# Kernel optimization log

Measured on AMD Instinct MI355X. Metric: run time of the kernel, lower is better.

The kernel has to match this reference:

```python
import jax, jax.numpy as jnp
import numpy as np

HASHMAP_SIZES = [65536, 262144]
HASHMAP_DIM = 4
RESO = 2097152
OUTPUT_DIM = 48


def setup_inputs() -> dict:
    key = jax.random.key(0)
    k1, k2, k3, k4 = jax.random.split(key, 4)
    total = sum(HASHMAP_SIZES)
    # codes initialized uniform(-1, 1) as in torch.nn.init.uniform_
    codes = jax.random.uniform(k1, (total, HASHMAP_DIM), dtype=jnp.float32, minval=-1.0, maxval=1.0)
    # bias-free linear head: stored as [in, out] so forward is feats @ W
    fan_in = len(HASHMAP_SIZES) * HASHMAP_DIM
    W = jax.random.normal(k2, (fan_in, OUTPUT_DIM), dtype=jnp.float32) / np.sqrt(fan_in)
    map_65536 = jax.random.randint(k3, (RESO, HASHMAP_DIM), 0, 65536, dtype=jnp.int64) if jax.config.jax_enable_x64 else jax.random.randint(k3, (RESO, HASHMAP_DIM), 0, 65536, dtype=jnp.int32)
    map_262144 = jax.random.randint(k4, (RESO, HASHMAP_DIM), 0, 262144, dtype=jnp.int32)
    return {"codes": codes, "W": W, "map_65536": map_65536, "map_262144": map_262144}


def _gather_level(code, idx_map):
    # code: [size, dim]; idx_map: [reso, dim]; out[n, i] = code[idx_map[n, i], i]
    dim_idx = jnp.arange(code.shape[1])[None, :]  # [1, dim]
    return code[idx_map, dim_idx]  # [reso, dim]


def reference(codes, W, map_65536, map_262144):
    # split stacked codebook into per-level tables
    code0 = codes[: HASHMAP_SIZES[0]]                      # [65536, 4]
    code1 = codes[HASHMAP_SIZES[0] : HASHMAP_SIZES[0] + HASHMAP_SIZES[1]]  # [262144, 4]
    out0 = _gather_level(code0, map_65536)    # [RESO, 4]
    out1 = _gather_level(code1, map_262144)   # [RESO, 4]
    feats = jnp.concatenate([out0, out1], axis=1)  # [RESO, 8]
    return feats @ W  # [RESO, 48]
```

## Files before the change

### kernel.cpp

```cpp
#include <hip/hip_runtime.h>


#define RESO    2097152
#define OUT_DIM 48
#define LVL0    65536
#define LVL1    262144
#define NCODES  (LVL0 + LVL1)
#define BLK     192
#define TILE    256
#define NITER   16

typedef int            vi4 __attribute__((ext_vector_type(4)));
typedef float          vf4 __attribute__((ext_vector_type(4)));
typedef unsigned short vu4 __attribute__((ext_vector_type(4)));

static __device__ __forceinline__ unsigned short f2bf_rne(float x) {
    unsigned int u = __float_as_uint(x);
    u += 0x7fffu + ((u >> 16) & 1u);
    return (unsigned short)(u >> 16);
}
static __device__ __forceinline__ float bf2f(unsigned short h) {
    return __uint_as_float(((unsigned int)h) << 16);
}

__global__ __launch_bounds__(256) void convert_kernel(
    const float* __restrict__ codes, unsigned short* __restrict__ bf)
{
    const int i = blockIdx.x * 256 + threadIdx.x;
    const vf4 v = ((const vf4*)codes)[i];
    vu4 o;
    o.x = f2bf_rne(v.x); o.y = f2bf_rne(v.y);
    o.z = f2bf_rne(v.z); o.w = f2bf_rne(v.w);
    ((vu4*)bf)[i] = o;
}

__global__ __launch_bounds__(BLK) void gshash_bf16_kernel(
    const unsigned short* __restrict__ tab,
    const float* __restrict__ W,
    const vi4*   __restrict__ map0,
    const vi4*   __restrict__ map1,
    float*       __restrict__ out)
{
    __shared__ float feats[TILE * 8];

    const int t     = threadIdx.x;
    const int col4  = t % 12;
    const int rbase = t / 12;
    const size_t row0 = (size_t)blockIdx.x * TILE;

    vf4 Wv[8];
    #pragma unroll
    for (int k = 0; k < 8; ++k)
        Wv[k] = ((const vf4*)(W + k * OUT_DIM))[col4];

    const unsigned short* __restrict__ t1 = tab + LVL0 * 4;

    #pragma unroll
    for (int half = 0; half < 2; ++half) {
        const int r = half * BLK + t;
        if (half == 0 || t < TILE - BLK) {
            const vi4 m0 = __builtin_nontemporal_load(&map0[row0 + r]);
            const vi4 m1 = __builtin_nontemporal_load(&map1[row0 + r]);
            vf4 a, b;
            a.x = bf2f(tab[m0.x * 4 + 0]);
            a.y = bf2f(tab[m0.y * 4 + 1]);
            a.z = bf2f(tab[m0.z * 4 + 2]);
            a.w = bf2f(tab[m0.w * 4 + 3]);
            b.x = bf2f(t1[m1.x * 4 + 0]);
            b.y = bf2f(t1[m1.y * 4 + 1]);
            b.z = bf2f(t1[m1.z * 4 + 2]);
            b.w = bf2f(t1[m1.w * 4 + 3]);
            *(vf4*)&feats[r * 8]     = a;
            *(vf4*)&feats[r * 8 + 4] = b;
        }
    }

    __syncthreads();

    vf4* __restrict__ out4 = (vf4*)(out + row0 * OUT_DIM);

    #pragma unroll
    for (int j = 0; j < NITER; ++j) {
        const int r = j * 16 + rbase;
        const vf4 fa = *(const vf4*)&feats[r * 8];
        const vf4 fb = *(const vf4*)&feats[r * 8 + 4];

        vf4 acc = fa.x * Wv[0];
        acc += fa.y * Wv[1];
        acc += fa.z * Wv[2];
        acc += fa.w * Wv[3];
        acc += fb.x * Wv[4];
        acc += fb.y * Wv[5];
        acc += fb.z * Wv[6];
        acc += fb.w * Wv[7];

        __builtin_nontemporal_store(acc, &out4[j * BLK + t]);
    }
}

__global__ __launch_bounds__(BLK) void gshash_f32_kernel(
    const float* __restrict__ codes,
    const float* __restrict__ W,
    const vi4*   __restrict__ map0,
    const vi4*   __restrict__ map1,
    float*       __restrict__ out)
{
    __shared__ float feats[TILE * 8];
    const int t     = threadIdx.x;
    const int col4  = t % 12;
    const int rbase = t / 12;
    const size_t row0 = (size_t)blockIdx.x * TILE;

    vf4 Wv[8];
    #pragma unroll
    for (int k = 0; k < 8; ++k)
        Wv[k] = ((const vf4*)(W + k * OUT_DIM))[col4];

    const float* __restrict__ c1 = codes + LVL0 * 4;

    #pragma unroll
    for (int half = 0; half < 2; ++half) {
        const int r = half * BLK + t;
        if (half == 0 || t < TILE - BLK) {
            const vi4 m0 = __builtin_nontemporal_load(&map0[row0 + r]);
            const vi4 m1 = __builtin_nontemporal_load(&map1[row0 + r]);
            vf4 a, b;
            a.x = codes[m0.x * 4 + 0];
            a.y = codes[m0.y * 4 + 1];
            a.z = codes[m0.z * 4 + 2];
            a.w = codes[m0.w * 4 + 3];
            b.x = c1[m1.x * 4 + 0];
            b.y = c1[m1.y * 4 + 1];
            b.z = c1[m1.z * 4 + 2];
            b.w = c1[m1.w * 4 + 3];
            *(vf4*)&feats[r * 8]     = a;
            *(vf4*)&feats[r * 8 + 4] = b;
        }
    }
    __syncthreads();

    vf4* __restrict__ out4 = (vf4*)(out + row0 * OUT_DIM);
    #pragma unroll
    for (int j = 0; j < NITER; ++j) {
        const int r = j * 16 + rbase;
        const vf4 fa = *(const vf4*)&feats[r * 8];
        const vf4 fb = *(const vf4*)&feats[r * 8 + 4];
        vf4 acc = fa.x * Wv[0];
        acc += fa.y * Wv[1];
        acc += fa.z * Wv[2];
        acc += fa.w * Wv[3];
        acc += fb.x * Wv[4];
        acc += fb.y * Wv[5];
        acc += fb.z * Wv[6];
        acc += fb.w * Wv[7];
        __builtin_nontemporal_store(acc, &out4[j * BLK + t]);
    }
}

extern "C" void kernel_launch(void* const* d_in, const int* in_sizes, int n_in,
                              void* d_out, int out_size, void* d_ws, size_t ws_size,
                              hipStream_t stream) {
    const float* codes = (const float*)d_in[0];
    const float* W     = (const float*)d_in[1];
    const vi4*   map0  = (const vi4*)d_in[2];
    const vi4*   map1  = (const vi4*)d_in[3];
    float*       out   = (float*)d_out;

    const size_t tab_bytes = (size_t)NCODES * 4 * sizeof(unsigned short);
    const int    grid      = RESO / TILE;

    if (ws_size >= tab_bytes) {
        unsigned short* tab = (unsigned short*)d_ws;
        convert_kernel<<<NCODES / 256, 256, 0, stream>>>(codes, tab);
        gshash_bf16_kernel<<<grid, BLK, 0, stream>>>(tab, W, map0, map1, out);
    } else {
        gshash_f32_kernel<<<grid, BLK, 0, stream>>>(codes, W, map0, map1, out);
    }
}
```

Measured before the change: 164.8 us.

## Split fused gather+GEMV into separate gather and consume kernels via bf16 workspace

Splits the fused kernel into a gather kernel that batches four rows of hashed lookups per thread and writes packed bf16 features to workspace. A separate consume kernel then reads those features and does the 8x48 projection. The aim is to raise memory-level parallelism for the random gathers and decouple them from the output-write-heavy projection. The cost is an extra intermediate buffer written and re-read, plus an additional kernel launch. It also requires more workspace, otherwise it falls back to the f32 path.

After: 164.3 us. No clear change (-0.3%).

```diff
diff --git a/kernel.cpp b/kernel.cpp
--- a/kernel.cpp
+++ b/kernel.cpp
@@ -6,6 +6,8 @@
 #define LVL0    65536
 #define LVL1    262144
 #define NCODES  (LVL0 + LVL1)
+#define GBLK    256
+#define GRPT    4
 #define BLK     192
 #define TILE    256
 #define NITER   16
@@ -13,6 +15,7 @@
 typedef int            vi4 __attribute__((ext_vector_type(4)));
 typedef float          vf4 __attribute__((ext_vector_type(4)));
 typedef unsigned short vu4 __attribute__((ext_vector_type(4)));
+typedef unsigned short vu8 __attribute__((ext_vector_type(8)));
 
 static __device__ __forceinline__ unsigned short f2bf_rne(float x) {
     unsigned int u = __float_as_uint(x);
@@ -34,11 +37,42 @@
     ((vu4*)bf)[i] = o;
 }
 
-__global__ __launch_bounds__(BLK) void gshash_bf16_kernel(
+__global__ __launch_bounds__(GBLK) void gather_kernel(
     const unsigned short* __restrict__ tab,
+    const vi4* __restrict__ map0,
+    const vi4* __restrict__ map1,
+    vu8*       __restrict__ feats16)
+{
+    const int t = threadIdx.x;
+    const size_t base = (size_t)blockIdx.x * (GBLK * GRPT) + t;
+
+    vi4 m0[GRPT], m1[GRPT];
+    #pragma unroll
+    for (int j = 0; j < GRPT; ++j) {
+        m0[j] = __builtin_nontemporal_load(&map0[base + j * GBLK]);
+        m1[j] = __builtin_nontemporal_load(&map1[base + j * GBLK]);
+    }
+
+    const unsigned short* __restrict__ t1 = tab + LVL0 * 4;
+
+    #pragma unroll
+    for (int j = 0; j < GRPT; ++j) {
+        vu8 o;
+        o[0] = tab[m0[j].x * 4 + 0];
+        o[1] = tab[m0[j].y * 4 + 1];
+        o[2] = tab[m0[j].z * 4 + 2];
+        o[3] = tab[m0[j].w * 4 + 3];
+        o[4] = t1[m1[j].x * 4 + 0];
+        o[5] = t1[m1[j].y * 4 + 1];
+        o[6] = t1[m1[j].z * 4 + 2];
+        o[7] = t1[m1[j].w * 4 + 3];
+        __builtin_nontemporal_store(o, &feats16[base + j * GBLK]);
+    }
+}
+
+__global__ __launch_bounds__(BLK) void consume_kernel(
+    const vu8*   __restrict__ feats16,
     const float* __restrict__ W,
-    const vi4*   __restrict__ map0,
-    const vi4*   __restrict__ map1,
     float*       __restrict__ out)
 {
     __shared__ float feats[TILE * 8];
@@ -53,23 +87,14 @@
     for (int k = 0; k < 8; ++k)
         Wv[k] = ((const vf4*)(W + k * OUT_DIM))[col4];
 
-    const unsigned short* __restrict__ t1 = tab + LVL0 * 4;
-
     #pragma unroll
     for (int half = 0; half < 2; ++half) {
         const int r = half * BLK + t;
         if (half == 0 || t < TILE - BLK) {
-            const vi4 m0 = __builtin_nontemporal_load(&map0[row0 + r]);
-            const vi4 m1 = __builtin_nontemporal_load(&map1[row0 + r]);
+            const vu8 v = __builtin_nontemporal_load(&feats16[row0 + r]);
             vf4 a, b;
-            a.x = bf2f(tab[m0.x * 4 + 0]);
-            a.y = bf2f(tab[m0.y * 4 + 1]);
-            a.z = bf2f(tab[m0.z * 4 + 2]);
-            a.w = bf2f(tab[m0.w * 4 + 3]);
-            b.x = bf2f(t1[m1.x * 4 + 0]);
-            b.y = bf2f(t1[m1.y * 4 + 1]);
-            b.z = bf2f(t1[m1.z * 4 + 2]);
-            b.w = bf2f(t1[m1.w * 4 + 3]);
+            a.x = bf2f(v[0]); a.y = bf2f(v[1]); a.z = bf2f(v[2]); a.w = bf2f(v[3]);
+            b.x = bf2f(v[4]); b.y = bf2f(v[5]); b.z = bf2f(v[6]); b.w = bf2f(v[7]);
             *(vf4*)&feats[r * 8]     = a;
             *(vf4*)&feats[r * 8 + 4] = b;
         }
@@ -166,14 +191,16 @@
     const vi4*   map1  = (const vi4*)d_in[3];
     float*       out   = (float*)d_out;
 
-    const size_t tab_bytes = (size_t)NCODES * 4 * sizeof(unsigned short);
-    const int    grid      = RESO / TILE;
-
-    if (ws_size >= tab_bytes) {
-        unsigned short* tab = (unsigned short*)d_ws;
+    const size_t tab_bytes   = (size_t)NCODES * 4 * sizeof(unsigned short);
+    const size_t feats_bytes = (size_t)RESO * 8 * sizeof(unsigned short);
+
+    if (ws_size >= tab_bytes + feats_bytes) {
+        unsigned short* tab   = (unsigned short*)d_ws;
+        vu8*            feats = (vu8*)((char*)d_ws + tab_bytes);
         convert_kernel<<<NCODES / 256, 256, 0, stream>>>(codes, tab);
-        gshash_bf16_kernel<<<grid, BLK, 0, stream>>>(tab, W, map0, map1, out);
+        gather_kernel<<<RESO / (GBLK * GRPT), GBLK, 0, stream>>>(tab, map0, map1, feats);
+        consume_kernel<<<RESO / TILE, BLK, 0, stream>>>(feats, W, out);
     } else {
-        gshash_f32_kernel<<<grid, BLK, 0, stream>>>(codes, W, map0, map1, out);
-    }
-}
+        gshash_f32_kernel<<<RESO / TILE, BLK, 0, stream>>>(codes, W, map0, map1, out);
+    }
+}
```

## Process four tiles per block with double-buffered LDS gather/compute pipelining

Applied to the files above, without the earlier changes.

Each block now handles four consecutive tiles, prefetching the next tile's map loads and bf16 table gathers into registers while computing and storing the current tile from a double-buffered shared array. This aims to hide gather latency behind the output-store phase and amortize the W register loads across more rows. It cuts the grid to a quarter of the blocks, which lowers the number of independent blocks available for latency hiding, and raises register pressure from the held prefetch values.

After: 165.3 us. Within noise of the previous version (+0.3%).

```diff
diff --git a/kernel.cpp b/kernel.cpp
--- a/kernel.cpp
+++ b/kernel.cpp
@@ -4,11 +4,12 @@
 #define RESO    2097152
 #define OUT_DIM 48
 #define LVL0    65536
-#define LVL1    262144
-#define NCODES  (LVL0 + LVL1)
+#define NCODES  327680
 #define BLK     192
 #define TILE    256
 #define NITER   16
+#define TPB     4
+#define NBLK    (RESO / (TILE * TPB))
 
 typedef int            vi4 __attribute__((ext_vector_type(4)));
 typedef float          vf4 __attribute__((ext_vector_type(4)));
@@ -34,19 +35,18 @@
     ((vu4*)bf)[i] = o;
 }
 
-__global__ __launch_bounds__(BLK) void gshash_bf16_kernel(
+__global__ __launch_bounds__(BLK) void gshash_pipe_kernel(
     const unsigned short* __restrict__ tab,
     const float* __restrict__ W,
     const vi4*   __restrict__ map0,
     const vi4*   __restrict__ map1,
     float*       __restrict__ out)
 {
-    __shared__ float feats[TILE * 8];
+    __shared__ float feats[2][TILE * 8];
 
     const int t     = threadIdx.x;
     const int col4  = t % 12;
     const int rbase = t / 12;
-    const size_t row0 = (size_t)blockIdx.x * TILE;
 
     vf4 Wv[8];
     #pragma unroll
@@ -54,48 +54,78 @@
         Wv[k] = ((const vf4*)(W + k * OUT_DIM))[col4];
 
     const unsigned short* __restrict__ t1 = tab + LVL0 * 4;
-
-    #pragma unroll
-    for (int half = 0; half < 2; ++half) {
-        const int r = half * BLK + t;
-        if (half == 0 || t < TILE - BLK) {
-            const vi4 m0 = __builtin_nontemporal_load(&map0[row0 + r]);
-            const vi4 m1 = __builtin_nontemporal_load(&map1[row0 + r]);
-            vf4 a, b;
-            a.x = bf2f(tab[m0.x * 4 + 0]);
-            a.y = bf2f(tab[m0.y * 4 + 1]);
-            a.z = bf2f(tab[m0.z * 4 + 2]);
-            a.w = bf2f(tab[m0.w * 4 + 3]);
-            b.x = bf2f(t1[m1.x * 4 + 0]);
-            b.y = bf2f(t1[m1.y * 4 + 1]);
-            b.z = bf2f(t1[m1.z * 4 + 2]);
-            b.w = bf2f(t1[m1.w * 4 + 3]);
-            *(vf4*)&feats[r * 8]     = a;
-            *(vf4*)&feats[r * 8 + 4] = b;
+    const size_t tile0 = (size_t)blockIdx.x * TPB;
+
+    vf4 pa0, pb0, pa1, pb1;
+
+    #define GATHER(row0)                                                     \
+    {                                                                        \
+        const vi4 m0 = __builtin_nontemporal_load(&map0[(row0) + t]);        \
+        const vi4 m1 = __builtin_nontemporal_load(&map1[(row0) + t]);        \
+        pa0.x = bf2f(tab[m0.x * 4 + 0]);                                     \
+        pa0.y = bf2f(tab[m0.y * 4 + 1]);                                     \
+        pa0.z = bf2f(tab[m0.z * 4 + 2]);                                     \
+        pa0.w = bf2f(tab[m0.w * 4 + 3]);                                     \
+        pb0.x = bf2f(t1[m1.x * 4 + 0]);                                      \
+        pb0.y = bf2f(t1[m1.y * 4 + 1]);                                      \
+        pb0.z = bf2f(t1[m1.z * 4 + 2]);                                      \
+        pb0.w = bf2f(t1[m1.w * 4 + 3]);                                      \
+        if (t < TILE - BLK) {                                                \
+            const vi4 n0 = __builtin_nontemporal_load(&map0[(row0) + BLK + t]); \
+            const vi4 n1 = __builtin_nontemporal_load(&map1[(row0) + BLK + t]); \
+            pa1.x = bf2f(tab[n0.x * 4 + 0]);                                 \
+            pa1.y = bf2f(tab[n0.y * 4 + 1]);                                 \
+            pa1.z = bf2f(tab[n0.z * 4 + 2]);                                 \
+            pa1.w = bf2f(tab[n0.w * 4 + 3]);                                 \
+            pb1.x = bf2f(t1[n1.x * 4 + 0]);                                  \
+            pb1.y = bf2f(t1[n1.y * 4 + 1]);                                  \
+            pb1.z = bf2f(t1[n1.z * 4 + 2]);                                  \
+            pb1.w = bf2f(t1[n1.w * 4 + 3]);                                  \
+        }                                                                    \
+    }
+
+    #define LDS_WRITE(buf)                                                   \
+    {                                                                        \
+        *(vf4*)&feats[buf][t * 8]     = pa0;                                 \
+        *(vf4*)&feats[buf][t * 8 + 4] = pb0;                                 \
+        if (t < TILE - BLK) {                                                \
+            *(vf4*)&feats[buf][(BLK + t) * 8]     = pa1;                     \
+            *(vf4*)&feats[buf][(BLK + t) * 8 + 4] = pb1;                     \
+        }                                                                    \
+    }
+
+    GATHER(tile0 * TILE);
+    LDS_WRITE(0);
+
+    #pragma unroll
+    for (int tl = 0; tl < TPB; ++tl) {
+        const int cur = tl & 1;
+
+        if (tl + 1 < TPB) GATHER((tile0 + tl + 1) * TILE);
+
+        __syncthreads();
+
+        vf4* __restrict__ out4 = (vf4*)(out + (tile0 + tl) * TILE * OUT_DIM);
+        #pragma unroll
+        for (int j = 0; j < NITER; ++j) {
+            const int r = j * 16 + rbase;
+            const vf4 fa = *(const vf4*)&feats[cur][r * 8];
+            const vf4 fb = *(const vf4*)&feats[cur][r * 8 + 4];
+            vf4 acc = fa.x * Wv[0];
+            acc += fa.y * Wv[1];
+            acc += fa.z * Wv[2];
+            acc += fa.w * Wv[3];
+            acc += fb.x * Wv[4];
+            acc += fb.y * Wv[5];
+            acc += fb.z * Wv[6];
+            acc += fb.w * Wv[7];
+            __builtin_nontemporal_store(acc, &out4[j * BLK + t]);
         }
-    }
-
-    __syncthreads();
-
-    vf4* __restrict__ out4 = (vf4*)(out + row0 * OUT_DIM);
-
-    #pragma unroll
-    for (int j = 0; j < NITER; ++j) {
-        const int r = j * 16 + rbase;
-        const vf4 fa = *(const vf4*)&feats[r * 8];
-        const vf4 fb = *(const vf4*)&feats[r * 8 + 4];
-
-        vf4 acc = fa.x * Wv[0];
-        acc += fa.y * Wv[1];
-        acc += fa.z * Wv[2];
-        acc += fa.w * Wv[3];
-        acc += fb.x * Wv[4];
-        acc += fb.y * Wv[5];
-        acc += fb.z * Wv[6];
-        acc += fb.w * Wv[7];
-
-        __builtin_nontemporal_store(acc, &out4[j * BLK + t]);
-    }
+
+        if (tl + 1 < TPB) LDS_WRITE(cur ^ 1);
+    }
+    #undef GATHER
+    #undef LDS_WRITE
 }
 
 __global__ __launch_bounds__(BLK) void gshash_f32_kernel(
@@ -117,7 +147,6 @@
         Wv[k] = ((const vf4*)(W + k * OUT_DIM))[col4];
 
     const float* __restrict__ c1 = codes + LVL0 * 4;
-
     #pragma unroll
     for (int half = 0; half < 2; ++half) {
         const int r = half * BLK + t;
@@ -167,13 +196,12 @@
     float*       out   = (float*)d_out;
 
     const size_t tab_bytes = (size_t)NCODES * 4 * sizeof(unsigned short);
-    const int    grid      = RESO / TILE;
 
     if (ws_size >= tab_bytes) {
         unsigned short* tab = (unsigned short*)d_ws;
         convert_kernel<<<NCODES / 256, 256, 0, stream>>>(codes, tab);
-        gshash_bf16_kernel<<<grid, BLK, 0, stream>>>(tab, W, map0, map1, out);
+        gshash_pipe_kernel<<<NBLK, BLK, 0, stream>>>(tab, W, map0, map1, out);
     } else {
-        gshash_f32_kernel<<<grid, BLK, 0, stream>>>(codes, W, map0, map1, out);
-    }
-}
+        gshash_f32_kernel<<<RESO / TILE, BLK, 0, stream>>>(codes, W, map0, map1, out);
+    }
+}
```

## Software-pipeline map loads and gathers across four tiles per block with double-buffered LDS

Applied to the files above, without the earlier changes.

Each block now processes four 256-row tiles instead of one. Index maps are prefetched two tiles ahead and gathers run one tile ahead, into a double-buffered shared-memory feature array, while the current tile's output is computed and stored. The aim is to hide gather latency behind the output-store phase and to amortize the W register loads per block. In exchange, register pressure rises, the grid shrinks by four, and parallelism from block-level scheduling drops.

Measured after the change: 148.8 us. 1.11x faster.

```diff
diff --git a/kernel.cpp b/kernel.cpp
--- a/kernel.cpp
+++ b/kernel.cpp
@@ -4,11 +4,12 @@
 #define RESO    2097152
 #define OUT_DIM 48
 #define LVL0    65536
-#define LVL1    262144
-#define NCODES  (LVL0 + LVL1)
+#define NCODES  327680
 #define BLK     192
 #define TILE    256
 #define NITER   16
+#define TPB     4
+#define NBLK    (RESO / (TILE * TPB))
 
 typedef int            vi4 __attribute__((ext_vector_type(4)));
 typedef float          vf4 __attribute__((ext_vector_type(4)));
@@ -34,19 +35,18 @@
     ((vu4*)bf)[i] = o;
 }
 
-__global__ __launch_bounds__(BLK) void gshash_bf16_kernel(
+__global__ __launch_bounds__(BLK) void gshash_pipe_kernel(
     const unsigned short* __restrict__ tab,
     const float* __restrict__ W,
     const vi4*   __restrict__ map0,
     const vi4*   __restrict__ map1,
     float*       __restrict__ out)
 {
-    __shared__ float feats[TILE * 8];
+    __shared__ float feats[2][TILE * 8];
 
     const int t     = threadIdx.x;
     const int col4  = t % 12;
     const int rbase = t / 12;
-    const size_t row0 = (size_t)blockIdx.x * TILE;
 
     vf4 Wv[8];
     #pragma unroll
@@ -54,48 +54,92 @@
         Wv[k] = ((const vf4*)(W + k * OUT_DIM))[col4];
 
     const unsigned short* __restrict__ t1 = tab + LVL0 * 4;
-
-    #pragma unroll
-    for (int half = 0; half < 2; ++half) {
-        const int r = half * BLK + t;
-        if (half == 0 || t < TILE - BLK) {
-            const vi4 m0 = __builtin_nontemporal_load(&map0[row0 + r]);
-            const vi4 m1 = __builtin_nontemporal_load(&map1[row0 + r]);
-            vf4 a, b;
-            a.x = bf2f(tab[m0.x * 4 + 0]);
-            a.y = bf2f(tab[m0.y * 4 + 1]);
-            a.z = bf2f(tab[m0.z * 4 + 2]);
-            a.w = bf2f(tab[m0.w * 4 + 3]);
-            b.x = bf2f(t1[m1.x * 4 + 0]);
-            b.y = bf2f(t1[m1.y * 4 + 1]);
-            b.z = bf2f(t1[m1.z * 4 + 2]);
-            b.w = bf2f(t1[m1.w * 4 + 3]);
-            *(vf4*)&feats[r * 8]     = a;
-            *(vf4*)&feats[r * 8 + 4] = b;
+    const size_t row00 = (size_t)blockIdx.x * (TPB * TILE);
+
+    vi4 m0b[2], m1b[2], n0b[2], n1b[2];
+    unsigned short g[16];
+
+    #define LOADMAPS(j, s) {                                                  \
+        const size_t r0 = row00 + (size_t)(j) * TILE;                         \
+        m0b[s] = __builtin_nontemporal_load(&map0[r0 + t]);                   \
+        m1b[s] = __builtin_nontemporal_load(&map1[r0 + t]);                   \
+        if (t < TILE - BLK) {                                                 \
+            n0b[s] = __builtin_nontemporal_load(&map0[r0 + BLK + t]);         \
+            n1b[s] = __builtin_nontemporal_load(&map1[r0 + BLK + t]);         \
+        } }
+
+    #define GATHERS(s) {                                                      \
+        g[0] = tab[m0b[s].x * 4 + 0];                                         \
+        g[1] = tab[m0b[s].y * 4 + 1];                                         \
+        g[2] = tab[m0b[s].z * 4 + 2];                                         \
+        g[3] = tab[m0b[s].w * 4 + 3];                                         \
+        g[4] = t1[m1b[s].x * 4 + 0];                                          \
+        g[5] = t1[m1b[s].y * 4 + 1];                                          \
+        g[6] = t1[m1b[s].z * 4 + 2];                                          \
+        g[7] = t1[m1b[s].w * 4 + 3];                                          \
+        if (t < TILE - BLK) {                                                 \
+            g[8]  = tab[n0b[s].x * 4 + 0];                                    \
+            g[9]  = tab[n0b[s].y * 4 + 1];                                    \
+            g[10] = tab[n0b[s].z * 4 + 2];                                    \
+            g[11] = tab[n0b[s].w * 4 + 3];                                    \
+            g[12] = t1[n1b[s].x * 4 + 0];                                     \
+            g[13] = t1[n1b[s].y * 4 + 1];                                     \
+            g[14] = t1[n1b[s].z * 4 + 2];                                     \
+            g[15] = t1[n1b[s].w * 4 + 3];                                     \
+        } }
+
+    #define LDSWRITE(buf) {                                                   \
+        vf4 a, b;                                                             \
+        a.x = bf2f(g[0]); a.y = bf2f(g[1]); a.z = bf2f(g[2]); a.w = bf2f(g[3]); \
+        b.x = bf2f(g[4]); b.y = bf2f(g[5]); b.z = bf2f(g[6]); b.w = bf2f(g[7]); \
+        *(vf4*)&feats[buf][t * 8]     = a;                                    \
+        *(vf4*)&feats[buf][t * 8 + 4] = b;                                    \
+        if (t < TILE - BLK) {                                                 \
+            vf4 c, d;                                                         \
+            c.x = bf2f(g[8]);  c.y = bf2f(g[9]);  c.z = bf2f(g[10]); c.w = bf2f(g[11]); \
+            d.x = bf2f(g[12]); d.y = bf2f(g[13]); d.z = bf2f(g[14]); d.w = bf2f(g[15]); \
+            *(vf4*)&feats[buf][(BLK + t) * 8]     = c;                        \
+            *(vf4*)&feats[buf][(BLK + t) * 8 + 4] = d;                        \
+        } }
+
+    LOADMAPS(0, 0);
+    LOADMAPS(1, 1);
+    GATHERS(0);
+    LDSWRITE(0);
+    __syncthreads();
+
+    #pragma unroll
+    for (int i = 0; i < TPB; ++i) {
+        const int cur = i & 1;
+
+        if (i + 2 < TPB) LOADMAPS(i + 2, cur);
+        if (i + 1 < TPB) GATHERS(cur ^ 1);
+
+        vf4* __restrict__ out4 = (vf4*)(out + (row00 + (size_t)i * TILE) * OUT_DIM);
+        #pragma unroll
+        for (int j = 0; j < NITER; ++j) {
+            const int r = j * 16 + rbase;
+            const vf4 fa = *(const vf4*)&feats[cur][r * 8];
+            const vf4 fb = *(const vf4*)&feats[cur][r * 8 + 4];
+            vf4 acc = fa.x * Wv[0];
+            acc += fa.y * Wv[1];
+            acc += fa.z * Wv[2];
+            acc += fa.w * Wv[3];
+            acc += fb.x * Wv[4];
+            acc += fb.y * Wv[5];
+            acc += fb.z * Wv[6];
+            acc += fb.w * Wv[7];
+            __builtin_nontemporal_store(acc, &out4[j * BLK + t]);
         }
-    }
-
-    __syncthreads();
-
-    vf4* __restrict__ out4 = (vf4*)(out + row0 * OUT_DIM);
-
-    #pragma unroll
-    for (int j = 0; j < NITER; ++j) {
-        const int r = j * 16 + rbase;
-        const vf4 fa = *(const vf4*)&feats[r * 8];
-        const vf4 fb = *(const vf4*)&feats[r * 8 + 4];
-
-        vf4 acc = fa.x * Wv[0];
-        acc += fa.y * Wv[1];
-        acc += fa.z * Wv[2];
-        acc += fa.w * Wv[3];
-        acc += fb.x * Wv[4];
-        acc += fb.y * Wv[5];
-        acc += fb.z * Wv[6];
-        acc += fb.w * Wv[7];
-
-        __builtin_nontemporal_store(acc, &out4[j * BLK + t]);
-    }
+
+        if (i + 1 < TPB) {
+            LDSWRITE(cur ^ 1);
+            __syncthreads();
+        }
+    }
+    #undef LOADMAPS
+    #undef GATHERS
+    #undef LDSWRITE
 }
 
 __global__ __launch_bounds__(BLK) void gshash_f32_kernel(
@@ -117,7 +161,6 @@
         Wv[k] = ((const vf4*)(W + k * OUT_DIM))[col4];
 
     const float* __restrict__ c1 = codes + LVL0 * 4;
-
     #pragma unroll
     for (int half = 0; half < 2; ++half) {
         const int r = half * BLK + t;
@@ -167,13 +210,12 @@
     float*       out   = (float*)d_out;
 
     const size_t tab_bytes = (size_t)NCODES * 4 * sizeof(unsigned short);
-    const int    grid      = RESO / TILE;
 
     if (ws_size >= tab_bytes) {
         unsigned short* tab = (unsigned short*)d_ws;
         convert_kernel<<<NCODES / 256, 256, 0, stream>>>(codes, tab);
-        gshash_bf16_kernel<<<grid, BLK, 0, stream>>>(tab, W, map0, map1, out);
+        gshash_pipe_kernel<<<NBLK, BLK, 0, stream>>>(tab, W, map0, map1, out);
     } else {
-        gshash_f32_kernel<<<grid, BLK, 0, stream>>>(codes, W, map0, map1, out);
-    }
-}
+        gshash_f32_kernel<<<RESO / TILE, BLK, 0, stream>>>(codes, W, map0, map1, out);
+    }
+}
```
